# Performance work log

Measured on AMD Instinct MI355X. Metric: run time of the kernel, lower is better.

## Reference

```python
import jax, jax.numpy as jnp
import numpy as np

B, S, H = 128, 512, 512  # batch, seq_len, hidden_units; feature dim is 2H = 1024
D = 2 * H


def setup_inputs() -> dict:
    key = jax.random.key(0)
    ks = jax.random.split(key, 8)
    scale = 1.0 / np.sqrt(D)
    return {
        "h_dec": jax.random.normal(ks[0], (1, B, H), jnp.float32),
        "c_dec": jax.random.normal(ks[1], (1, B, H), jnp.float32),
        "encoder_output": jax.random.normal(ks[2], (B, S, D), jnp.float32),
        "x_padding_masks": jnp.ones((B, S), jnp.float32),
        "coverage_vector": jax.random.uniform(ks[3], (B, S), jnp.float32),
        "Wh_w": jax.random.normal(ks[4], (D, D), jnp.float32) * scale,
        "Ws_w": jax.random.normal(ks[5], (D, D), jnp.float32) * scale,
        "Ws_b": jax.random.normal(ks[6], (D,), jnp.float32) * scale,
        "v_w": jax.random.normal(ks[7], (D,), jnp.float32) * scale,
        "wc_w": jax.random.normal(jax.random.fold_in(key, 99), (D,), jnp.float32) * scale,
    }


def reference(h_dec, c_dec, encoder_output, x_padding_masks, coverage_vector,
              Wh_w, Ws_w, Ws_b, v_w, wc_w):
    # s_t: concat(h, c) -> (B, 2H)
    s_t = jnp.concatenate([h_dec[0], c_dec[0]], axis=-1)  # (B, D)
    enc_feat = jnp.einsum('bsd,ed->bse', encoder_output, Wh_w)       # Wh(enc)
    dec_feat = s_t @ Ws_w.T + Ws_b                                    # (B, D)
    cov_feat = coverage_vector[:, :, None] * wc_w[None, None, :]      # w_c(cov)
    att_inputs = enc_feat + dec_feat[:, None, :] + cov_feat           # (B, S, D)
    score = jnp.tanh(att_inputs) @ v_w                                # (B, S)
    aw = jax.nn.softmax(score, axis=1) * x_padding_masks              # masked softmax
    aw = aw / jnp.sum(aw, axis=1, keepdims=True)                      # renormalize
    context_vector = jnp.einsum('bs,bsd->bd', aw, encoder_output)     # (B, D)
    new_coverage = coverage_vector + aw
    return context_vector, aw, new_coverage
```

## Files before the change

### kernel.cpp

```cpp
#include <hip/hip_runtime.h>
#include <hip/hip_bf16.h>
#include <cstdint>
#include <cstddef>


typedef __attribute__((ext_vector_type(8))) short bf16x8;
typedef __attribute__((ext_vector_type(4))) float f32x4;

#define GLOBAL_AS(p) ((const __attribute__((address_space(1))) unsigned int*)(p))
#define LDS_AS(p)    ((__attribute__((address_space(3))) unsigned int*)(p))

__device__ __forceinline__ short f2bf(float f) {
    union { float f; uint32_t u; } v; v.f = f;
    uint32_t u = v.u + 0x7fffu + ((v.u >> 16) & 1u);
    return (short)(u >> 16);
}

__device__ __forceinline__ float bf2f(short s) {
    union { uint32_t u; float f; } v; v.u = ((uint32_t)(uint16_t)s) << 16;
    return v.f;
}

__device__ __forceinline__ bf16x8 cvt8(float4 a, float4 b) {
    bf16x8 r;
    r[0] = f2bf(a.x); r[1] = f2bf(a.y); r[2] = f2bf(a.z); r[3] = f2bf(a.w);
    r[4] = f2bf(b.x); r[5] = f2bf(b.y); r[6] = f2bf(b.z); r[7] = f2bf(b.w);
    return r;
}

__device__ __forceinline__ float fast_tanh(float x) {
    x = fminf(10.f, fmaxf(-10.f, x));
    float e = __expf(2.f * x);
    return (e - 1.f) / (e + 1.f);
}

__device__ __forceinline__ float fast_tanh2(float x) {
    float e = __builtin_amdgcn_exp2f(x * 2.885390081777927f);
    return 1.f - 2.f * __builtin_amdgcn_rcpf(e + 1.f);
}

__global__ __launch_bounds__(256) void cvt_plus_dec(
    const float* __restrict__ enc, const float* __restrict__ Wh,
    short* __restrict__ enc_bf, short* __restrict__ Wh_bf,
    const float* __restrict__ hd, const float* __restrict__ cd,
    const float* __restrict__ Ws, float* __restrict__ dec_part)
{
    __shared__ __align__(16) short As[128 * 40];
    __shared__ __align__(16) short Bs[128 * 40];
    const int t = threadIdx.x;

    if (blockIdx.x < 33280) {
        size_t i = ((size_t)blockIdx.x * 256 + t) * 8;
        const float* src; short* dst; size_t off;
        const size_t NE = 67108864;
        if (i < NE) { src = enc; dst = enc_bf; off = i; }
        else        { src = Wh;  dst = Wh_bf;  off = i - NE; }
        float4 a = *(const float4*)(src + off);
        float4 b = *(const float4*)(src + off + 4);
        *(bf16x8*)(dst + off) = cvt8(a, b);
        return;
    }

    const int bid = blockIdx.x - 33280;
    const int bx = bid & 7;
    const int kc = bid >> 3;
    const int wv = t >> 6, lane = t & 63, q = lane >> 4, c = lane & 15;
    const int wm = wv & 1, wn = wv >> 1;
    const int ar = t >> 1, ah = t & 1;

    const float* abase = ((kc < 2) ? hd : cd) + (size_t)ar * 512 + (kc & 1) * 256 + ah * 16;
    const float* bbase = Ws + ((size_t)(bx * 128 + ar)) * 1024 + kc * 256 + ah * 16;
    short* awr = &As[ar * 40 + ah * 16];
    short* bwr = &Bs[ar * 40 + ah * 16];

    f32x4 acc[4][4];
#pragma unroll
    for (int i = 0; i < 4; ++i)
#pragma unroll
        for (int j = 0; j < 4; ++j) acc[i][j] = (f32x4){0.f, 0.f, 0.f, 0.f};

    for (int k0 = 0; k0 < 256; k0 += 32) {
        const float4* ap = (const float4*)(abase + k0);
        const float4* bp = (const float4*)(bbase + k0);
        float4 a0 = ap[0], a1 = ap[1], a2 = ap[2], a3 = ap[3];
        float4 b0 = bp[0], b1 = bp[1], b2 = bp[2], b3 = bp[3];
        *(bf16x8*)awr = cvt8(a0, a1);
        *(bf16x8*)(awr + 8) = cvt8(a2, a3);
        *(bf16x8*)bwr = cvt8(b0, b1);
        *(bf16x8*)(bwr + 8) = cvt8(b2, b3);
        __syncthreads();
        bf16x8 af[4], bf[4];
#pragma unroll
        for (int i = 0; i < 4; ++i) af[i] = *(const bf16x8*)&As[(wm * 64 + i * 16 + c) * 40 + q * 8];
#pragma unroll
        for (int j = 0; j < 4; ++j) bf[j] = *(const bf16x8*)&Bs[(wn * 64 + j * 16 + c) * 40 + q * 8];
#pragma unroll
        for (int i = 0; i < 4; ++i)
#pragma unroll
            for (int j = 0; j < 4; ++j)
                acc[i][j] = __builtin_amdgcn_mfma_f32_16x16x32_bf16(af[i], bf[j], acc[i][j], 0, 0, 0);
        __syncthreads();
    }

    const int n0 = bx * 128 + wn * 64;
    float* dp = dec_part + (size_t)kc * 131072;
#pragma unroll
    for (int i = 0; i < 4; ++i)
#pragma unroll
        for (int rr = 0; rr < 4; ++rr) {
            int bidx = wm * 64 + i * 16 + q * 4 + rr;
#pragma unroll
            for (int j = 0; j < 4; ++j)
                dp[(size_t)bidx * 1024 + n0 + j * 16 + c] = acc[i][j][rr];
        }
}


#define BARRIER() do { asm volatile("" ::: "memory"); \
    __builtin_amdgcn_s_barrier(); asm volatile("" ::: "memory"); } while (0)
#define WAIT_LGKM0() do { asm volatile("s_waitcnt lgkmcnt(0)" ::: "memory"); \
    __builtin_amdgcn_sched_barrier(0); } while (0)
#define STAGE(gp, kcol, arr, bufks, a) \
    __builtin_amdgcn_global_load_lds(GLOBAL_AS((gp) + (kcol)), \
        LDS_AS(&(arr)[(bufks) * 8192 + (a) * 4096 + wst]), 16, 0, 0)

__global__ __launch_bounds__(512, 2) void attn_score_gemm8(
    const short* __restrict__ encb, const short* __restrict__ Whb,
    const float* __restrict__ dec_part, const float* __restrict__ Wsb,
    const float* __restrict__ cov,
    const float* __restrict__ wc_w, const float* __restrict__ v_w,
    float* __restrict__ p_part)
{
    __shared__ __align__(16) short SA[32768];
    __shared__ __align__(16) short SB[32768];

    const int tid = threadIdx.x;
    const int wv = tid >> 6, lane = tid & 63, q = lane >> 4, c = lane & 15;
    const int wm = wv >> 2, wn = wv & 3;

    const int lin = blockIdx.x;
    const int xcd = lin & 7;
    const int idx = lin >> 3;
    const int bx  = idx & 3;
    const int my  = xcd * 32 + (idx >> 2);
    const int m0  = my * 256;
    const int n0  = bx * 256;
    const int b   = my >> 1;
    const int s0c = (my & 1) * 256;

    const int srow = tid >> 2;
    const int SLOT = ((tid & 3) ^ ((tid >> 3) & 3)) * 8;
    const short* gA0 = encb + (size_t)(m0 + srow) * 1024 + SLOT;
    const short* gA1 = gA0 + 131072;
    const short* gB0 = Whb + (size_t)(n0 + srow) * 1024 + SLOT;
    const short* gB1 = gB0 + 131072;
    const int wst = wv * 512;

    const int sq = (q ^ ((c >> 1) & 3)) * 8;
    int aoff[8], boff[4];
#pragma unroll
    for (int i = 0; i < 8; ++i) aoff[i] = (wm * 128 + i * 16 + c) * 32 + sq;
#pragma unroll
    for (int j = 0; j < 4; ++j) boff[j] = (wn * 64 + j * 16 + c) * 32 + sq;

    f32x4 acc[8][4];
#pragma unroll
    for (int i = 0; i < 8; ++i)
#pragma unroll
        for (int j = 0; j < 4; ++j) acc[i][j] = (f32x4){0.f, 0.f, 0.f, 0.f};

    STAGE(gA0,  0, SA, 0, 0);  STAGE(gA1,  0, SA, 0, 1);
    STAGE(gB0,  0, SB, 0, 0);  STAGE(gB1,  0, SB, 0, 1);
    STAGE(gA0, 32, SA, 1, 0);  STAGE(gA1, 32, SA, 1, 1);
    STAGE(gB0, 32, SB, 1, 0);  STAGE(gB1, 32, SB, 1, 1);
    STAGE(gA0, 64, SA, 2, 0);  STAGE(gA1, 64, SA, 2, 1);
    STAGE(gB0, 64, SB, 2, 0);  STAGE(gB1, 64, SB, 2, 1);
    asm volatile("s_waitcnt vmcnt(4)" ::: "memory");
    __builtin_amdgcn_s_barrier();
    asm volatile("" ::: "memory");

#pragma unroll 2
    for (int t = 0; t < 16; ++t) {
        const int cur = t & 1, nxt = cur ^ 1;
        const int kc = t * 64;
        const short* A0 = &SA[cur * 16384];
        const short* A1 = A0 + 8192;
        const short* B0 = &SB[cur * 16384];
        const short* B1 = B0 + 8192;

        bf16x8 af[4], bfr[4];

#pragma unroll
        for (int i = 0; i < 4; ++i) af[i] = *(const bf16x8*)&A0[aoff[i]];
#pragma unroll
        for (int j = 0; j < 4; ++j) bfr[j] = *(const bf16x8*)&B0[boff[j]];
        if (t < 15) { STAGE(gA0, kc + 96, SA, nxt * 2 + 1, 0);
                      STAGE(gA1, kc + 96, SA, nxt * 2 + 1, 1); }
        WAIT_LGKM0();
        __builtin_amdgcn_s_setprio(1);
#pragma unroll
        for (int i = 0; i < 4; ++i)
#pragma unroll
            for (int j = 0; j < 4; ++j)
                acc[i][j] = __builtin_amdgcn_mfma_f32_16x16x32_bf16(af[i], bfr[j], acc[i][j], 0, 0, 0);
        __builtin_amdgcn_s_setprio(0);

#pragma unroll
        for (int i = 0; i < 4; ++i) af[i] = *(const bf16x8*)&A0[aoff[4 + i]];
        if (t < 15) { STAGE(gB0, kc + 96, SB, nxt * 2 + 1, 0);
                      STAGE(gB1, kc + 96, SB, nxt * 2 + 1, 1); }
        WAIT_LGKM0();
        __builtin_amdgcn_s_setprio(1);
#pragma unroll
        for (int i = 0; i < 4; ++i)
#pragma unroll
            for (int j = 0; j < 4; ++j)
                acc[4 + i][j] = __builtin_amdgcn_mfma_f32_16x16x32_bf16(af[i], bfr[j], acc[4 + i][j], 0, 0, 0);
        __builtin_amdgcn_s_setprio(0);
        BARRIER();

#pragma unroll
        for (int i = 0; i < 4; ++i) af[i] = *(const bf16x8*)&A1[aoff[i]];
#pragma unroll
        for (int j = 0; j < 4; ++j) bfr[j] = *(const bf16x8*)&B1[boff[j]];
        if (t < 14) { STAGE(gA0, kc + 128, SA, cur * 2, 0);
                      STAGE(gA1, kc + 128, SA, cur * 2, 1); }
        WAIT_LGKM0();
        __builtin_amdgcn_s_setprio(1);
#pragma unroll
        for (int i = 0; i < 4; ++i)
#pragma unroll
            for (int j = 0; j < 4; ++j)
                acc[i][j] = __builtin_amdgcn_mfma_f32_16x16x32_bf16(af[i], bfr[j], acc[i][j], 0, 0, 0);
        __builtin_amdgcn_s_setprio(0);

#pragma unroll
        for (int i = 0; i < 4; ++i) af[i] = *(const bf16x8*)&A1[aoff[4 + i]];
        if (t < 14) { STAGE(gB0, kc + 128, SB, cur * 2, 0);
                      STAGE(gB1, kc + 128, SB, cur * 2, 1); }
        WAIT_LGKM0();
        __builtin_amdgcn_s_setprio(1);
#pragma unroll
        for (int i = 0; i < 4; ++i)
#pragma unroll
            for (int j = 0; j < 4; ++j)
                acc[4 + i][j] = __builtin_amdgcn_mfma_f32_16x16x32_bf16(af[i], bfr[j], acc[4 + i][j], 0, 0, 0);
        __builtin_amdgcn_s_setprio(0);
        if (t <= 13) asm volatile("s_waitcnt vmcnt(4)" ::: "memory");
        else         asm volatile("s_waitcnt vmcnt(0)" ::: "memory");
        __builtin_amdgcn_s_barrier();
        asm volatile("" ::: "memory");
    }

    const int eb = n0 + wn * 64;
    float v_e[4], wc_e[4], dec_e[4];
#pragma unroll
    for (int j = 0; j < 4; ++j) {
        int e = eb + j * 16 + c;
        v_e[j]  = v_w[e];
        wc_e[j] = wc_w[e];
        float d = Wsb[e];
#pragma unroll
        for (int p = 0; p < 4; ++p) d += dec_part[(size_t)p * 131072 + (size_t)b * 1024 + e];
        dec_e[j] = d;
    }
    const float* covb = cov + (size_t)b * 512 + s0c;
    float* pp = p_part + (size_t)(bx * 4 + wn) * 65536 + (size_t)my * 256;
#pragma unroll
    for (int i = 0; i < 8; ++i)
#pragma unroll
        for (int rr = 0; rr < 4; ++rr) {
            int r = wm * 128 + i * 16 + q * 4 + rr;
            float cs = covb[r];
            float p = 0.f;
#pragma unroll
            for (int j = 0; j < 4; ++j) {
                float att = acc[i][j][rr] + dec_e[j] + cs * wc_e[j];
                p += v_e[j] * fast_tanh2(att);
            }
            p += __shfl_xor(p, 1);
            p += __shfl_xor(p, 2);
            p += __shfl_xor(p, 4);
            p += __shfl_xor(p, 8);
            if (c == 0) pp[r] = p;
        }
}

__global__ __launch_bounds__(256) void attn_score_gemm_fb(
    const float* __restrict__ enc, const short* __restrict__ Wh,
    const float* __restrict__ dec_feat, const float* __restrict__ cov,
    const float* __restrict__ wc_w, const float* __restrict__ v_w,
    float* __restrict__ p_part)
{
    __shared__ __align__(16) short As[128 * 40];
    __shared__ __align__(16) short Bs[128 * 40];
    const int t = threadIdx.x;
    const int bx = blockIdx.x;
    const int by = blockIdx.y;
    const int b  = by >> 2;
    const int s0 = (by & 3) * 128;

    const int wv = t >> 6, lane = t & 63, q = lane >> 4, c = lane & 15;
    const int wm = wv & 1, wn = wv >> 1;
    const int ar = t >> 1, ah = t & 1;

    const float* aptr = enc + ((size_t)(by * 128 + ar)) * 1024 + ah * 16;
    const short* bptr = Wh + ((size_t)(bx * 128 + ar)) * 1024 + ah * 16;
    short* awr = &As[ar * 40 + ah * 16];
    short* bwr = &Bs[ar * 40 + ah * 16];

    f32x4 acc[4][4];
#pragma unroll
    for (int i = 0; i < 4; ++i)
#pragma unroll
        for (int j = 0; j < 4; ++j) acc[i][j] = (f32x4){0.f, 0.f, 0.f, 0.f};

    for (int k0 = 0; k0 < 1024; k0 += 32) {
        const float4* ap = (const float4*)(aptr + k0);
        float4 a0 = ap[0], a1 = ap[1], a2 = ap[2], a3 = ap[3];
        bf16x8 bv0 = *(const bf16x8*)(bptr + k0);
        bf16x8 bv1 = *(const bf16x8*)(bptr + k0 + 8);
        *(bf16x8*)awr = cvt8(a0, a1);
        *(bf16x8*)(awr + 8) = cvt8(a2, a3);
        *(bf16x8*)bwr = bv0;
        *(bf16x8*)(bwr + 8) = bv1;
        __syncthreads();
        bf16x8 af[4], bf[4];
#pragma unroll
        for (int i = 0; i < 4; ++i) af[i] = *(const bf16x8*)&As[(wm * 64 + i * 16 + c) * 40 + q * 8];
#pragma unroll
        for (int j = 0; j < 4; ++j) bf[j] = *(const bf16x8*)&Bs[(wn * 64 + j * 16 + c) * 40 + q * 8];
#pragma unroll
        for (int i = 0; i < 4; ++i)
#pragma unroll
            for (int j = 0; j < 4; ++j)
                acc[i][j] = __builtin_amdgcn_mfma_f32_16x16x32_bf16(af[i], bf[j], acc[i][j], 0, 0, 0);
        __syncthreads();
    }

    const int n0 = bx * 128 + wn * 64;
    float v_e[4], wc_e[4], dec_e[4];
#pragma unroll
    for (int j = 0; j < 4; ++j) {
        int e = n0 + j * 16 + c;
        v_e[j]  = v_w[e];
        wc_e[j] = wc_w[e];
        dec_e[j] = dec_feat[(size_t)b * 1024 + e];
    }
    const float* covb = cov + (size_t)b * 512;
    float* pp = p_part + ((size_t)(bx * 2 + wn)) * 65536 + (size_t)b * 512;
#pragma unroll
    for (int i = 0; i < 4; ++i)
#pragma unroll
        for (int rr = 0; rr < 4; ++rr) {
            int s = s0 + wm * 64 + i * 16 + q * 4 + rr;
            float cs = covb[s];
            float p = 0.f;
#pragma unroll
            for (int j = 0; j < 4; ++j) {
                float att = acc[i][j][rr] + dec_e[j] + cs * wc_e[j];
                p += v_e[j] * fast_tanh(att);
            }
            p += __shfl_xor(p, 1);
            p += __shfl_xor(p, 2);
            p += __shfl_xor(p, 4);
            p += __shfl_xor(p, 8);
            if (c == 0) pp[s] = p;
        }
}

__global__ __launch_bounds__(256) void dec_gemm(
    const float* __restrict__ hd, const float* __restrict__ cd,
    const short* __restrict__ Ws, const float* __restrict__ Wsb,
    float* __restrict__ dec_feat)
{
    __shared__ __align__(16) short As[128 * 40];
    __shared__ __align__(16) short Bs[128 * 40];
    const int t = threadIdx.x;
    const int bx = blockIdx.x;
    const int wv = t >> 6, lane = t & 63, q = lane >> 4, c = lane & 15;
    const int wm = wv & 1, wn = wv >> 1;
    const int ar = t >> 1, ah = t & 1;

    const short* bptr = Ws + ((size_t)(bx * 128 + ar)) * 1024 + ah * 16;
    short* awr = &As[ar * 40 + ah * 16];
    short* bwr = &Bs[ar * 40 + ah * 16];

    f32x4 acc[4][4];
#pragma unroll
    for (int i = 0; i < 4; ++i)
#pragma unroll
        for (int j = 0; j < 4; ++j) acc[i][j] = (f32x4){0.f, 0.f, 0.f, 0.f};

    for (int k0 = 0; k0 < 1024; k0 += 32) {
        const int k = k0 + ah * 16;
        const float* src = (k < 512) ? (hd + (size_t)ar * 512 + k)
                                     : (cd + (size_t)ar * 512 + (k - 512));
        const float4* ap = (const float4*)src;
        float4 a0 = ap[0], a1 = ap[1], a2 = ap[2], a3 = ap[3];
        bf16x8 bv0 = *(const bf16x8*)(bptr + k0);
        bf16x8 bv1 = *(const bf16x8*)(bptr + k0 + 8);
        *(bf16x8*)awr = cvt8(a0, a1);
        *(bf16x8*)(awr + 8) = cvt8(a2, a3);
        *(bf16x8*)bwr = bv0;
        *(bf16x8*)(bwr + 8) = bv1;
        __syncthreads();
        bf16x8 af[4], bf[4];
#pragma unroll
        for (int i = 0; i < 4; ++i) af[i] = *(const bf16x8*)&As[(wm * 64 + i * 16 + c) * 40 + q * 8];
#pragma unroll
        for (int j = 0; j < 4; ++j) bf[j] = *(const bf16x8*)&Bs[(wn * 64 + j * 16 + c) * 40 + q * 8];
#pragma unroll
        for (int i = 0; i < 4; ++i)
#pragma unroll
            for (int j = 0; j < 4; ++j)
                acc[i][j] = __builtin_amdgcn_mfma_f32_16x16x32_bf16(af[i], bf[j], acc[i][j], 0, 0, 0);
        __syncthreads();
    }

    const int n0 = bx * 128 + wn * 64;
    float wsb_e[4];
#pragma unroll
    for (int j = 0; j < 4; ++j) wsb_e[j] = Wsb[n0 + j * 16 + c];
#pragma unroll
    for (int i = 0; i < 4; ++i)
#pragma unroll
        for (int rr = 0; rr < 4; ++rr) {
            int bidx = wm * 64 + i * 16 + q * 4 + rr;
#pragma unroll
            for (int j = 0; j < 4; ++j) {
                int e = n0 + j * 16 + c;
                dec_feat[(size_t)bidx * 1024 + e] = acc[i][j][rr] + wsb_e[j];
            }
        }
}

__global__ __launch_bounds__(512) void softmax_kernel(
    const float* __restrict__ p_part, int ns, const float* __restrict__ mask,
    const float* __restrict__ cov, float* __restrict__ aw, float* __restrict__ ncov)
{
    __shared__ float red[8];
    const int b = blockIdx.x, t = threadIdx.x;
    const int w = t >> 6, lane = t & 63;
    const size_t idx = (size_t)b * 512 + t;

    float sc = 0.f;
    for (int k = 0; k < ns; ++k) sc += p_part[(size_t)k * 65536 + idx];

    float m = sc;
#pragma unroll
    for (int o = 1; o < 64; o <<= 1) m = fmaxf(m, __shfl_xor(m, o));
    if (lane == 0) red[w] = m;
    __syncthreads();
#pragma unroll
    for (int i = 0; i < 8; ++i) m = fmaxf(m, red[i]);
    __syncthreads();

    float e = __expf(sc - m);
    float s = e;
#pragma unroll
    for (int o = 1; o < 64; o <<= 1) s += __shfl_xor(s, o);
    if (lane == 0) red[w] = s;
    __syncthreads();
    s = 0.f;
#pragma unroll
    for (int i = 0; i < 8; ++i) s += red[i];
    __syncthreads();

    float wv = (e / s) * mask[idx];
    float s2 = wv;
#pragma unroll
    for (int o = 1; o < 64; o <<= 1) s2 += __shfl_xor(s2, o);
    if (lane == 0) red[w] = s2;
    __syncthreads();
    s2 = 0.f;
#pragma unroll
    for (int i = 0; i < 8; ++i) s2 += red[i];

    float awv = wv / s2;
    aw[idx] = awv;
    ncov[idx] = cov[idx] + awv;
}

__global__ __launch_bounds__(256) void context_part(
    const short* __restrict__ encb, const float* __restrict__ aw, float* __restrict__ cpart)
{
    const int sc = blockIdx.x & 7;
    const int b  = blockIdx.x >> 3;
    const int t  = threadIdx.x;
    const int dl = t & 127;
    const int si = t >> 7;
    const short* ebase = encb + ((size_t)(b * 512 + sc * 64 + si)) * 1024 + dl * 8;
    const float* awp = aw + (size_t)b * 512 + sc * 64 + si;
    float acc[8];
#pragma unroll
    for (int i = 0; i < 8; ++i) acc[i] = 0.f;
#pragma unroll 16
    for (int s = 0; s < 64; s += 2) {
        float w = awp[s];
        bf16x8 e = *(const bf16x8*)(ebase + (size_t)s * 1024);
#pragma unroll
        for (int i = 0; i < 8; ++i) acc[i] += w * bf2f(e[i]);
    }
    float* cp = cpart + ((size_t)(sc * 2 + si) * 128 + b) * 1024 + dl * 8;
    *(float4*)(cp)     = (float4){acc[0], acc[1], acc[2], acc[3]};
    *(float4*)(cp + 4) = (float4){acc[4], acc[5], acc[6], acc[7]};
}

__global__ __launch_bounds__(256) void ctx_reduce(
    const float* __restrict__ cpart, float* __restrict__ ctx)
{
    int i = blockIdx.x * 256 + threadIdx.x;
    float s = 0.f;
#pragma unroll
    for (int k = 0; k < 16; ++k) s += cpart[(size_t)k * 131072 + i];
    ctx[i] = s;
}

__global__ __launch_bounds__(256) void context_f32(
    const float* __restrict__ enc, const float* __restrict__ aw, float* __restrict__ ctx)
{
    const int schunk = blockIdx.x;
    const int b = blockIdx.y;
    const int t = threadIdx.x;
    const float* ebase = enc + ((size_t)(b * 512 + schunk * 128)) * 1024 + t * 4;
    const float* awp = aw + (size_t)b * 512 + schunk * 128;
    float ax = 0.f, ay = 0.f, az = 0.f, aww = 0.f;
#pragma unroll 4
    for (int s = 0; s < 128; ++s) {
        float w = awp[s];
        float4 e4 = *(const float4*)(ebase + (size_t)s * 1024);
        ax += w * e4.x; ay += w * e4.y; az += w * e4.z; aww += w * e4.w;
    }
    float* cp = ctx + (size_t)b * 1024 + t * 4;
    atomicAdd(cp + 0, ax);
    atomicAdd(cp + 1, ay);
    atomicAdd(cp + 2, az);
    atomicAdd(cp + 3, aww);
}

__global__ void cvt_f32_bf16(const float* __restrict__ src, short* __restrict__ dst, int n) {
    int i = (blockIdx.x * 256 + threadIdx.x) * 4;
    if (i < n) {
        float4 f = *(const float4*)(src + i);
        short4 o;
        o.x = f2bf(f.x); o.y = f2bf(f.y); o.z = f2bf(f.z); o.w = f2bf(f.w);
        *(short4*)(dst + i) = o;
    }
}

extern "C" void kernel_launch(void* const* d_in, const int* in_sizes, int n_in,
                              void* d_out, int out_size, void* d_ws, size_t ws_size,
                              hipStream_t stream) {
    const float* hd   = (const float*)d_in[0];
    const float* cd   = (const float*)d_in[1];
    const float* enc  = (const float*)d_in[2];
    const float* mask = (const float*)d_in[3];
    const float* cov  = (const float*)d_in[4];
    const float* Wh   = (const float*)d_in[5];
    const float* Ws   = (const float*)d_in[6];
    const float* Wsb  = (const float*)d_in[7];
    const float* vw   = (const float*)d_in[8];
    const float* wcw  = (const float*)d_in[9];

    float* out  = (float*)d_out;
    float* ctx  = out;
    float* aw   = out + 131072;
    float* ncov = out + 196608;

    char* ws = (char*)d_ws;
    float* p_part   = (float*)ws;
    float* dec_part = (float*)(ws + (4u << 20));
    short* Wh_bf    = (short*)(ws + (6u << 20));
    short* enc_bf   = (short*)(ws + (8u << 20));
    float* cpart    = (float*)ws;
    const size_t need_big = (8ull << 20) + (128ull << 20);

    if (ws_size >= need_big) {
        cvt_plus_dec<<<33312, 256, 0, stream>>>(enc, Wh, enc_bf, Wh_bf, hd, cd, Ws, dec_part);
        attn_score_gemm8<<<1024, 512, 0, stream>>>(enc_bf, Wh_bf, dec_part, Wsb, cov, wcw, vw, p_part);
        softmax_kernel<<<128, 512, 0, stream>>>(p_part, 16, mask, cov, aw, ncov);
        context_part<<<1024, 256, 0, stream>>>(enc_bf, aw, cpart);
        ctx_reduce<<<512, 256, 0, stream>>>(cpart, ctx);
    } else {
        float* p_part16 = (float*)ws;
        float* dec_feat = (float*)(ws + (4u << 20));
        short* Wh_bf2   = (short*)(ws + (4u << 20) + (512u << 10));
        short* Ws_bf    = (short*)(ws + (6u << 20) + (512u << 10));
        hipMemsetAsync(ctx, 0, 128 * 1024 * sizeof(float), stream);
        cvt_f32_bf16<<<1024, 256, 0, stream>>>(Wh, Wh_bf2, 1024 * 1024);
        cvt_f32_bf16<<<1024, 256, 0, stream>>>(Ws, Ws_bf, 1024 * 1024);
        dec_gemm<<<8, 256, 0, stream>>>(hd, cd, Ws_bf, Wsb, dec_feat);
        attn_score_gemm_fb<<<dim3(8, 512), 256, 0, stream>>>(enc, Wh_bf2, dec_feat, cov, wcw, vw, p_part16);
        softmax_kernel<<<128, 512, 0, stream>>>(p_part16, 16, mask, cov, aw, ncov);
        context_f32<<<dim3(4, 128), 256, 0, stream>>>(enc, aw, ctx);
    }
}
```

Before: 583.5 us.

## Replace 4-stage LDS pipeline with simple double buffer to raise occupancy

Rewrites the main score GEMM loop from a 4-slot, 64-wide k-step pipeline with interleaved half-stages into a plain double buffer over 32-wide k-slices, with one barrier per slice. LDS use per block is halved and launch bounds ask for 4 blocks per CU instead of 2, aiming to hide latency through more resident waves rather than deep software prefetch. In exchange each iteration waits for all outstanding global loads (vmcnt(0)) before its barrier, so there is less prefetch depth and more barriers. With 8x4 f32x4 accumulators per thread, the register cap implied by 4 blocks of 512 threads may cause spills.

```diff
diff --git a/kernel.cpp b/kernel.cpp
--- a/kernel.cpp
+++ b/kernel.cpp
@@ -116,23 +116,21 @@
 }
 
 
-#define BARRIER() do { asm volatile("" ::: "memory"); \
-    __builtin_amdgcn_s_barrier(); asm volatile("" ::: "memory"); } while (0)
 #define WAIT_LGKM0() do { asm volatile("s_waitcnt lgkmcnt(0)" ::: "memory"); \
     __builtin_amdgcn_sched_barrier(0); } while (0)
-#define STAGE(gp, kcol, arr, bufks, a) \
+#define STAGE9(gp, kcol, arr, slot, a) \
     __builtin_amdgcn_global_load_lds(GLOBAL_AS((gp) + (kcol)), \
-        LDS_AS(&(arr)[(bufks) * 8192 + (a) * 4096 + wst]), 16, 0, 0)
-
-__global__ __launch_bounds__(512, 2) void attn_score_gemm8(
+        LDS_AS(&(arr)[(slot) * 8192 + (a) * 4096 + wst]), 16, 0, 0)
+
+__global__ __launch_bounds__(512, 4) void attn_score_gemm9(
     const short* __restrict__ encb, const short* __restrict__ Whb,
     const float* __restrict__ dec_part, const float* __restrict__ Wsb,
     const float* __restrict__ cov,
     const float* __restrict__ wc_w, const float* __restrict__ v_w,
     float* __restrict__ p_part)
 {
-    __shared__ __align__(16) short SA[32768];
-    __shared__ __align__(16) short SB[32768];
+    __shared__ __align__(16) short SA[16384];
+    __shared__ __align__(16) short SB[16384];
 
     const int tid = threadIdx.x;
     const int wv = tid >> 6, lane = tid & 63, q = lane >> 4, c = lane & 15;
@@ -169,85 +167,36 @@
 #pragma unroll
         for (int j = 0; j < 4; ++j) acc[i][j] = (f32x4){0.f, 0.f, 0.f, 0.f};
 
-    STAGE(gA0,  0, SA, 0, 0);  STAGE(gA1,  0, SA, 0, 1);
-    STAGE(gB0,  0, SB, 0, 0);  STAGE(gB1,  0, SB, 0, 1);
-    STAGE(gA0, 32, SA, 1, 0);  STAGE(gA1, 32, SA, 1, 1);
-    STAGE(gB0, 32, SB, 1, 0);  STAGE(gB1, 32, SB, 1, 1);
-    STAGE(gA0, 64, SA, 2, 0);  STAGE(gA1, 64, SA, 2, 1);
-    STAGE(gB0, 64, SB, 2, 0);  STAGE(gB1, 64, SB, 2, 1);
-    asm volatile("s_waitcnt vmcnt(4)" ::: "memory");
+    STAGE9(gA0, 0, SA, 0, 0);  STAGE9(gA1, 0, SA, 0, 1);
+    STAGE9(gB0, 0, SB, 0, 0);  STAGE9(gB1, 0, SB, 0, 1);
+    asm volatile("s_waitcnt vmcnt(0)" ::: "memory");
     __builtin_amdgcn_s_barrier();
     asm volatile("" ::: "memory");
 
 #pragma unroll 2
-    for (int t = 0; t < 16; ++t) {
-        const int cur = t & 1, nxt = cur ^ 1;
-        const int kc = t * 64;
-        const short* A0 = &SA[cur * 16384];
-        const short* A1 = A0 + 8192;
-        const short* B0 = &SB[cur * 16384];
-        const short* B1 = B0 + 8192;
-
-        bf16x8 af[4], bfr[4];
-
-#pragma unroll
-        for (int i = 0; i < 4; ++i) af[i] = *(const bf16x8*)&A0[aoff[i]];
-#pragma unroll
-        for (int j = 0; j < 4; ++j) bfr[j] = *(const bf16x8*)&B0[boff[j]];
-        if (t < 15) { STAGE(gA0, kc + 96, SA, nxt * 2 + 1, 0);
-                      STAGE(gA1, kc + 96, SA, nxt * 2 + 1, 1); }
+    for (int kh = 0; kh < 32; ++kh) {
+        const int slot = kh & 1, nslot = slot ^ 1;
+        if (kh < 31) {
+            const int kcol = (kh + 1) * 32;
+            STAGE9(gA0, kcol, SA, nslot, 0);  STAGE9(gA1, kcol, SA, nslot, 1);
+            STAGE9(gB0, kcol, SB, nslot, 0);  STAGE9(gB1, kcol, SB, nslot, 1);
+        }
+        const short* A = &SA[slot * 8192];
+        const short* B = &SB[slot * 8192];
+        bf16x8 af[8], bfr[4];
+#pragma unroll
+        for (int i = 0; i < 8; ++i) af[i] = *(const bf16x8*)&A[aoff[i]];
+#pragma unroll
+        for (int j = 0; j < 4; ++j) bfr[j] = *(const bf16x8*)&B[boff[j]];
         WAIT_LGKM0();
         __builtin_amdgcn_s_setprio(1);
 #pragma unroll
-        for (int i = 0; i < 4; ++i)
+        for (int i = 0; i < 8; ++i)
 #pragma unroll
             for (int j = 0; j < 4; ++j)
                 acc[i][j] = __builtin_amdgcn_mfma_f32_16x16x32_bf16(af[i], bfr[j], acc[i][j], 0, 0, 0);
         __builtin_amdgcn_s_setprio(0);
-
-#pragma unroll
-        for (int i = 0; i < 4; ++i) af[i] = *(const bf16x8*)&A0[aoff[4 + i]];
-        if (t < 15) { STAGE(gB0, kc + 96, SB, nxt * 2 + 1, 0);
-                      STAGE(gB1, kc + 96, SB, nxt * 2 + 1, 1); }
-        WAIT_LGKM0();
-        __builtin_amdgcn_s_setprio(1);
-#pragma unroll
-        for (int i = 0; i < 4; ++i)
-#pragma unroll
-            for (int j = 0; j < 4; ++j)
-                acc[4 + i][j] = __builtin_amdgcn_mfma_f32_16x16x32_bf16(af[i], bfr[j], acc[4 + i][j], 0, 0, 0);
-        __builtin_amdgcn_s_setprio(0);
-        BARRIER();
-
-#pragma unroll
-        for (int i = 0; i < 4; ++i) af[i] = *(const bf16x8*)&A1[aoff[i]];
-#pragma unroll
-        for (int j = 0; j < 4; ++j) bfr[j] = *(const bf16x8*)&B1[boff[j]];
-        if (t < 14) { STAGE(gA0, kc + 128, SA, cur * 2, 0);
-                      STAGE(gA1, kc + 128, SA, cur * 2, 1); }
-        WAIT_LGKM0();
-        __builtin_amdgcn_s_setprio(1);
-#pragma unroll
-        for (int i = 0; i < 4; ++i)
-#pragma unroll
-            for (int j = 0; j < 4; ++j)
-                acc[i][j] = __builtin_amdgcn_mfma_f32_16x16x32_bf16(af[i], bfr[j], acc[i][j], 0, 0, 0);
-        __builtin_amdgcn_s_setprio(0);
-
-#pragma unroll
-        for (int i = 0; i < 4; ++i) af[i] = *(const bf16x8*)&A1[aoff[4 + i]];
-        if (t < 14) { STAGE(gB0, kc + 128, SB, cur * 2, 0);
-                      STAGE(gB1, kc + 128, SB, cur * 2, 1); }
-        WAIT_LGKM0();
-        __builtin_amdgcn_s_setprio(1);
-#pragma unroll
-        for (int i = 0; i < 4; ++i)
-#pragma unroll
-            for (int j = 0; j < 4; ++j)
-                acc[4 + i][j] = __builtin_amdgcn_mfma_f32_16x16x32_bf16(af[i], bfr[j], acc[4 + i][j], 0, 0, 0);
-        __builtin_amdgcn_s_setprio(0);
-        if (t <= 13) asm volatile("s_waitcnt vmcnt(4)" ::: "memory");
-        else         asm volatile("s_waitcnt vmcnt(0)" ::: "memory");
+        asm volatile("s_waitcnt vmcnt(0)" ::: "memory");
         __builtin_amdgcn_s_barrier();
         asm volatile("" ::: "memory");
     }
@@ -578,7 +527,7 @@
 
     if (ws_size >= need_big) {
         cvt_plus_dec<<<33312, 256, 0, stream>>>(enc, Wh, enc_bf, Wh_bf, hd, cd, Ws, dec_part);
-        attn_score_gemm8<<<1024, 512, 0, stream>>>(enc_bf, Wh_bf, dec_part, Wsb, cov, wcw, vw, p_part);
+        attn_score_gemm9<<<1024, 512, 0, stream>>>(enc_bf, Wh_bf, dec_part, Wsb, cov, wcw, vw, p_part);
         softmax_kernel<<<128, 512, 0, stream>>>(p_part, 16, mask, cov, aw, ncov);
         context_part<<<1024, 256, 0, stream>>>(enc_bf, aw, cpart);
         ctx_reduce<<<512, 256, 0, stream>>>(cpart, ctx);
```

Result: slower. 1.839 ms (+215.1%).

## Fuse encoder fp32-to-bf16 conversion into score GEMM A-tile loading

Applied to the files above, without the earlier changes.

Drops the separate pass that converted the whole encoder tensor to bf16 in workspace. The score GEMM now loads fp32 encoder rows into registers, converts them, and writes bf16 to LDS inside its software pipeline, while the B tiles still use direct global-to-LDS loads. The context kernel now reads the fp32 encoder directly. This avoids writing and re-reading a 128MB bf16 copy and reduces workspace needs, but doubles the A-operand global traffic in the GEMM, adds conversion ALU work and register pressure, and changes the pipeline's wait and barrier structure.

```diff
diff --git a/kernel.cpp b/kernel.cpp
--- a/kernel.cpp
+++ b/kernel.cpp
@@ -39,9 +39,8 @@
     return 1.f - 2.f * __builtin_amdgcn_rcpf(e + 1.f);
 }
 
-__global__ __launch_bounds__(256) void cvt_plus_dec(
-    const float* __restrict__ enc, const float* __restrict__ Wh,
-    short* __restrict__ enc_bf, short* __restrict__ Wh_bf,
+__global__ __launch_bounds__(256) void dec_cvt(
+    const float* __restrict__ Wh, short* __restrict__ Wh_bf,
     const float* __restrict__ hd, const float* __restrict__ cd,
     const float* __restrict__ Ws, float* __restrict__ dec_part)
 {
@@ -49,19 +48,15 @@
     __shared__ __align__(16) short Bs[128 * 40];
     const int t = threadIdx.x;
 
-    if (blockIdx.x < 33280) {
+    if (blockIdx.x < 512) {
         size_t i = ((size_t)blockIdx.x * 256 + t) * 8;
-        const float* src; short* dst; size_t off;
-        const size_t NE = 67108864;
-        if (i < NE) { src = enc; dst = enc_bf; off = i; }
-        else        { src = Wh;  dst = Wh_bf;  off = i - NE; }
-        float4 a = *(const float4*)(src + off);
-        float4 b = *(const float4*)(src + off + 4);
-        *(bf16x8*)(dst + off) = cvt8(a, b);
+        float4 a = *(const float4*)(Wh + i);
+        float4 b = *(const float4*)(Wh + i + 4);
+        *(bf16x8*)(Wh_bf + i) = cvt8(a, b);
         return;
     }
 
-    const int bid = blockIdx.x - 33280;
+    const int bid = blockIdx.x - 512;
     const int bx = bid & 7;
     const int kc = bid >> 3;
     const int wv = t >> 6, lane = t & 63, q = lane >> 4, c = lane & 15;
@@ -116,16 +111,14 @@
 }
 
 
-#define BARRIER() do { asm volatile("" ::: "memory"); \
-    __builtin_amdgcn_s_barrier(); asm volatile("" ::: "memory"); } while (0)
 #define WAIT_LGKM0() do { asm volatile("s_waitcnt lgkmcnt(0)" ::: "memory"); \
     __builtin_amdgcn_sched_barrier(0); } while (0)
 #define STAGE(gp, kcol, arr, bufks, a) \
     __builtin_amdgcn_global_load_lds(GLOBAL_AS((gp) + (kcol)), \
         LDS_AS(&(arr)[(bufks) * 8192 + (a) * 4096 + wst]), 16, 0, 0)
 
-__global__ __launch_bounds__(512, 2) void attn_score_gemm8(
-    const short* __restrict__ encb, const short* __restrict__ Whb,
+__global__ __launch_bounds__(512, 2) void attn_score_gemm11(
+    const float* __restrict__ encf, const short* __restrict__ Whb,
     const float* __restrict__ dec_part, const float* __restrict__ Wsb,
     const float* __restrict__ cov,
     const float* __restrict__ wc_w, const float* __restrict__ v_w,
@@ -150,12 +143,17 @@
 
     const int srow = tid >> 2;
     const int SLOT = ((tid & 3) ^ ((tid >> 3) & 3)) * 8;
-    const short* gA0 = encb + (size_t)(m0 + srow) * 1024 + SLOT;
-    const short* gA1 = gA0 + 131072;
     const short* gB0 = Whb + (size_t)(n0 + srow) * 1024 + SLOT;
     const short* gB1 = gB0 + 131072;
     const int wst = wv * 512;
 
+    const int ar2 = tid >> 1;
+    const int as2 = (tid & 1) * 2;
+    const int ag  = as2 ^ ((ar2 >> 1) & 3);
+    const float* gAf  = encf + (size_t)(m0 + ar2) * 1024 + ag * 8;
+    const float* gAf2 = encf + (size_t)(m0 + ar2) * 1024 + (ag ^ 1) * 8;
+    const int wrA = ar2 * 32 + as2 * 8;
+
     const int sq = (q ^ ((c >> 1) & 3)) * 8;
     int aoff[8], boff[4];
 #pragma unroll
@@ -169,20 +167,31 @@
 #pragma unroll
         for (int j = 0; j < 4; ++j) acc[i][j] = (f32x4){0.f, 0.f, 0.f, 0.f};
 
-    STAGE(gA0,  0, SA, 0, 0);  STAGE(gA1,  0, SA, 0, 1);
+    float4 aR0, aR1, aR2, aR3, aR4, aR5, aR6, aR7;
+    aR0 = *(const float4*)(gAf);        aR1 = *(const float4*)(gAf + 4);
+    aR2 = *(const float4*)(gAf2);       aR3 = *(const float4*)(gAf2 + 4);
+    aR4 = *(const float4*)(gAf + 32);   aR5 = *(const float4*)(gAf + 36);
+    aR6 = *(const float4*)(gAf2 + 32);  aR7 = *(const float4*)(gAf2 + 36);
     STAGE(gB0,  0, SB, 0, 0);  STAGE(gB1,  0, SB, 0, 1);
-    STAGE(gA0, 32, SA, 1, 0);  STAGE(gA1, 32, SA, 1, 1);
     STAGE(gB0, 32, SB, 1, 0);  STAGE(gB1, 32, SB, 1, 1);
-    STAGE(gA0, 64, SA, 2, 0);  STAGE(gA1, 64, SA, 2, 1);
-    STAGE(gB0, 64, SB, 2, 0);  STAGE(gB1, 64, SB, 2, 1);
     asm volatile("s_waitcnt vmcnt(4)" ::: "memory");
+    {
+        short* w0 = &SA[wrA];
+        *(bf16x8*)w0        = cvt8(aR0, aR1);
+        *(bf16x8*)(w0 + 8)  = cvt8(aR2, aR3);
+        short* w1 = w0 + 8192;
+        *(bf16x8*)w1        = cvt8(aR4, aR5);
+        *(bf16x8*)(w1 + 8)  = cvt8(aR6, aR7);
+    }
+    asm volatile("s_waitcnt vmcnt(0)" ::: "memory");
+    asm volatile("s_waitcnt lgkmcnt(0)" ::: "memory");
     __builtin_amdgcn_s_barrier();
     asm volatile("" ::: "memory");
 
 #pragma unroll 2
     for (int t = 0; t < 16; ++t) {
         const int cur = t & 1, nxt = cur ^ 1;
-        const int kc = t * 64;
+        const int kb = (t + 1) * 64;
         const short* A0 = &SA[cur * 16384];
         const short* A1 = A0 + 8192;
         const short* B0 = &SB[cur * 16384];
@@ -194,8 +203,12 @@
         for (int i = 0; i < 4; ++i) af[i] = *(const bf16x8*)&A0[aoff[i]];
 #pragma unroll
         for (int j = 0; j < 4; ++j) bfr[j] = *(const bf16x8*)&B0[boff[j]];
-        if (t < 15) { STAGE(gA0, kc + 96, SA, nxt * 2 + 1, 0);
-                      STAGE(gA1, kc + 96, SA, nxt * 2 + 1, 1); }
+        if (t < 15) {
+            aR0 = *(const float4*)(gAf + kb);        aR1 = *(const float4*)(gAf + kb + 4);
+            aR2 = *(const float4*)(gAf2 + kb);       aR3 = *(const float4*)(gAf2 + kb + 4);
+            aR4 = *(const float4*)(gAf + kb + 32);   aR5 = *(const float4*)(gAf + kb + 36);
+            aR6 = *(const float4*)(gAf2 + kb + 32);  aR7 = *(const float4*)(gAf2 + kb + 36);
+        }
         WAIT_LGKM0();
         __builtin_amdgcn_s_setprio(1);
 #pragma unroll
@@ -207,8 +220,12 @@
 
 #pragma unroll
         for (int i = 0; i < 4; ++i) af[i] = *(const bf16x8*)&A0[aoff[4 + i]];
-        if (t < 15) { STAGE(gB0, kc + 96, SB, nxt * 2 + 1, 0);
-                      STAGE(gB1, kc + 96, SB, nxt * 2 + 1, 1); }
+        if (t < 15) {
+            STAGE(gB0, kb,      SB, nxt * 2,     0);
+            STAGE(gB1, kb,      SB, nxt * 2,     1);
+            STAGE(gB0, kb + 32, SB, nxt * 2 + 1, 0);
+            STAGE(gB1, kb + 32, SB, nxt * 2 + 1, 1);
+        }
         WAIT_LGKM0();
         __builtin_amdgcn_s_setprio(1);
 #pragma unroll
@@ -217,14 +234,20 @@
             for (int j = 0; j < 4; ++j)
                 acc[4 + i][j] = __builtin_amdgcn_mfma_f32_16x16x32_bf16(af[i], bfr[j], acc[4 + i][j], 0, 0, 0);
         __builtin_amdgcn_s_setprio(0);
-        BARRIER();
 
 #pragma unroll
         for (int i = 0; i < 4; ++i) af[i] = *(const bf16x8*)&A1[aoff[i]];
 #pragma unroll
         for (int j = 0; j < 4; ++j) bfr[j] = *(const bf16x8*)&B1[boff[j]];
-        if (t < 14) { STAGE(gA0, kc + 128, SA, cur * 2, 0);
-                      STAGE(gA1, kc + 128, SA, cur * 2, 1); }
+        if (t < 15) {
+            asm volatile("s_waitcnt vmcnt(4)" ::: "memory");
+            short* w0 = &SA[nxt * 16384 + wrA];
+            *(bf16x8*)w0        = cvt8(aR0, aR1);
+            *(bf16x8*)(w0 + 8)  = cvt8(aR2, aR3);
+            short* w1 = w0 + 8192;
+            *(bf16x8*)w1        = cvt8(aR4, aR5);
+            *(bf16x8*)(w1 + 8)  = cvt8(aR6, aR7);
+        }
         WAIT_LGKM0();
         __builtin_amdgcn_s_setprio(1);
 #pragma unroll
@@ -236,8 +259,6 @@
 
 #pragma unroll
         for (int i = 0; i < 4; ++i) af[i] = *(const bf16x8*)&A1[aoff[4 + i]];
-        if (t < 14) { STAGE(gB0, kc + 128, SB, cur * 2, 0);
-                      STAGE(gB1, kc + 128, SB, cur * 2, 1); }
         WAIT_LGKM0();
         __builtin_amdgcn_s_setprio(1);
 #pragma unroll
@@ -246,8 +267,7 @@
             for (int j = 0; j < 4; ++j)
                 acc[4 + i][j] = __builtin_amdgcn_mfma_f32_16x16x32_bf16(af[i], bfr[j], acc[4 + i][j], 0, 0, 0);
         __builtin_amdgcn_s_setprio(0);
-        if (t <= 13) asm volatile("s_waitcnt vmcnt(4)" ::: "memory");
-        else         asm volatile("s_waitcnt vmcnt(0)" ::: "memory");
+        asm volatile("s_waitcnt vmcnt(0)" ::: "memory");
         __builtin_amdgcn_s_barrier();
         asm volatile("" ::: "memory");
     }
@@ -284,6 +304,89 @@
             p += __shfl_xor(p, 8);
             if (c == 0) pp[r] = p;
         }
+}
+
+__global__ __launch_bounds__(512) void softmax_kernel(
+    const float* __restrict__ p_part, int ns, const float* __restrict__ mask,
+    const float* __restrict__ cov, float* __restrict__ aw, float* __restrict__ ncov)
+{
+    __shared__ float red[8];
+    const int b = blockIdx.x, t = threadIdx.x;
+    const int w = t >> 6, lane = t & 63;
+    const size_t idx = (size_t)b * 512 + t;
+
+    float sc = 0.f;
+    for (int k = 0; k < ns; ++k) sc += p_part[(size_t)k * 65536 + idx];
+
+    float m = sc;
+#pragma unroll
+    for (int o = 1; o < 64; o <<= 1) m = fmaxf(m, __shfl_xor(m, o));
+    if (lane == 0) red[w] = m;
+    __syncthreads();
+#pragma unroll
+    for (int i = 0; i < 8; ++i) m = fmaxf(m, red[i]);
+    __syncthreads();
+
+    float e = __expf(sc - m);
+    float s = e;
+#pragma unroll
+    for (int o = 1; o < 64; o <<= 1) s += __shfl_xor(s, o);
+    if (lane == 0) red[w] = s;
+    __syncthreads();
+    s = 0.f;
+#pragma unroll
+    for (int i = 0; i < 8; ++i) s += red[i];
+    __syncthreads();
+
+    float wv = (e / s) * mask[idx];
+    float s2 = wv;
+#pragma unroll
+    for (int o = 1; o < 64; o <<= 1) s2 += __shfl_xor(s2, o);
+    if (lane == 0) red[w] = s2;
+    __syncthreads();
+    s2 = 0.f;
+#pragma unroll
+    for (int i = 0; i < 8; ++i) s2 += red[i];
+
+    float awv = wv / s2;
+    aw[idx] = awv;
+    ncov[idx] = cov[idx] + awv;
+}
+
+__global__ __launch_bounds__(256) void context_part_f32(
+    const float* __restrict__ enc, const float* __restrict__ aw, float* __restrict__ cpart)
+{
+    const int sc = blockIdx.x & 7;
+    const int b  = blockIdx.x >> 3;
+    const int t  = threadIdx.x;
+    const int dl = t & 127;
+    const int si = t >> 7;
+    const float* ebase = enc + ((size_t)(b * 512 + sc * 64 + si)) * 1024 + dl * 8;
+    const float* awp = aw + (size_t)b * 512 + sc * 64 + si;
+    float acc[8];
+#pragma unroll
+    for (int i = 0; i < 8; ++i) acc[i] = 0.f;
+#pragma unroll 8
+    for (int s = 0; s < 64; s += 2) {
+        float w = awp[s];
+        float4 e0 = *(const float4*)(ebase + (size_t)s * 1024);
+        float4 e1 = *(const float4*)(ebase + (size_t)s * 1024 + 4);
+        acc[0] += w * e0.x; acc[1] += w * e0.y; acc[2] += w * e0.z; acc[3] += w * e0.w;
+        acc[4] += w * e1.x; acc[5] += w * e1.y; acc[6] += w * e1.z; acc[7] += w * e1.w;
+    }
+    float* cp = cpart + ((size_t)(sc * 2 + si) * 128 + b) * 1024 + dl * 8;
+    *(float4*)(cp)     = (float4){acc[0], acc[1], acc[2], acc[3]};
+    *(float4*)(cp + 4) = (float4){acc[4], acc[5], acc[6], acc[7]};
+}
+
+__global__ __launch_bounds__(256) void ctx_reduce(
+    const float* __restrict__ cpart, float* __restrict__ ctx)
+{
+    int i = blockIdx.x * 256 + threadIdx.x;
+    float s = 0.f;
+#pragma unroll
+    for (int k = 0; k < 16; ++k) s += cpart[(size_t)k * 131072 + i];
+    ctx[i] = s;
 }
 
 __global__ __launch_bounds__(256) void attn_score_gemm_fb(
@@ -435,88 +538,6 @@
         }
 }
 
-__global__ __launch_bounds__(512) void softmax_kernel(
-    const float* __restrict__ p_part, int ns, const float* __restrict__ mask,
-    const float* __restrict__ cov, float* __restrict__ aw, float* __restrict__ ncov)
-{
-    __shared__ float red[8];
-    const int b = blockIdx.x, t = threadIdx.x;
-    const int w = t >> 6, lane = t & 63;
-    const size_t idx = (size_t)b * 512 + t;
-
-    float sc = 0.f;
-    for (int k = 0; k < ns; ++k) sc += p_part[(size_t)k * 65536 + idx];
-
-    float m = sc;
-#pragma unroll
-    for (int o = 1; o < 64; o <<= 1) m = fmaxf(m, __shfl_xor(m, o));
-    if (lane == 0) red[w] = m;
-    __syncthreads();
-#pragma unroll
-    for (int i = 0; i < 8; ++i) m = fmaxf(m, red[i]);
-    __syncthreads();
-
-    float e = __expf(sc - m);
-    float s = e;
-#pragma unroll
-    for (int o = 1; o < 64; o <<= 1) s += __shfl_xor(s, o);
-    if (lane == 0) red[w] = s;
-    __syncthreads();
-    s = 0.f;
-#pragma unroll
-    for (int i = 0; i < 8; ++i) s += red[i];
-    __syncthreads();
-
-    float wv = (e / s) * mask[idx];
-    float s2 = wv;
-#pragma unroll
-    for (int o = 1; o < 64; o <<= 1) s2 += __shfl_xor(s2, o);
-    if (lane == 0) red[w] = s2;
-    __syncthreads();
-    s2 = 0.f;
-#pragma unroll
-    for (int i = 0; i < 8; ++i) s2 += red[i];
-
-    float awv = wv / s2;
-    aw[idx] = awv;
-    ncov[idx] = cov[idx] + awv;
-}
-
-__global__ __launch_bounds__(256) void context_part(
-    const short* __restrict__ encb, const float* __restrict__ aw, float* __restrict__ cpart)
-{
-    const int sc = blockIdx.x & 7;
-    const int b  = blockIdx.x >> 3;
-    const int t  = threadIdx.x;
-    const int dl = t & 127;
-    const int si = t >> 7;
-    const short* ebase = encb + ((size_t)(b * 512 + sc * 64 + si)) * 1024 + dl * 8;
-    const float* awp = aw + (size_t)b * 512 + sc * 64 + si;
-    float acc[8];
-#pragma unroll
-    for (int i = 0; i < 8; ++i) acc[i] = 0.f;
-#pragma unroll 16
-    for (int s = 0; s < 64; s += 2) {
-        float w = awp[s];
-        bf16x8 e = *(const bf16x8*)(ebase + (size_t)s * 1024);
-#pragma unroll
-        for (int i = 0; i < 8; ++i) acc[i] += w * bf2f(e[i]);
-    }
-    float* cp = cpart + ((size_t)(sc * 2 + si) * 128 + b) * 1024 + dl * 8;
-    *(float4*)(cp)     = (float4){acc[0], acc[1], acc[2], acc[3]};
-    *(float4*)(cp + 4) = (float4){acc[4], acc[5], acc[6], acc[7]};
-}
-
-__global__ __launch_bounds__(256) void ctx_reduce(
-    const float* __restrict__ cpart, float* __restrict__ ctx)
-{
-    int i = blockIdx.x * 256 + threadIdx.x;
-    float s = 0.f;
-#pragma unroll
-    for (int k = 0; k < 16; ++k) s += cpart[(size_t)k * 131072 + i];
-    ctx[i] = s;
-}
-
 __global__ __launch_bounds__(256) void context_f32(
     const float* __restrict__ enc, const float* __restrict__ aw, float* __restrict__ ctx)
 {
@@ -572,15 +593,14 @@
     float* p_part   = (float*)ws;
     float* dec_part = (float*)(ws + (4u << 20));
     short* Wh_bf    = (short*)(ws + (6u << 20));
-    short* enc_bf   = (short*)(ws + (8u << 20));
     float* cpart    = (float*)ws;
-    const size_t need_big = (8ull << 20) + (128ull << 20);
+    const size_t need_big = (16ull << 20);
 
     if (ws_size >= need_big) {
-        cvt_plus_dec<<<33312, 256, 0, stream>>>(enc, Wh, enc_bf, Wh_bf, hd, cd, Ws, dec_part);
-        attn_score_gemm8<<<1024, 512, 0, stream>>>(enc_bf, Wh_bf, dec_part, Wsb, cov, wcw, vw, p_part);
+        dec_cvt<<<544, 256, 0, stream>>>(Wh, Wh_bf, hd, cd, Ws, dec_part);
+        attn_score_gemm11<<<1024, 512, 0, stream>>>(enc, Wh_bf, dec_part, Wsb, cov, wcw, vw, p_part);
         softmax_kernel<<<128, 512, 0, stream>>>(p_part, 16, mask, cov, aw, ncov);
-        context_part<<<1024, 256, 0, stream>>>(enc_bf, aw, cpart);
+        context_part_f32<<<1024, 256, 0, stream>>>(enc, aw, cpart);
         ctx_reduce<<<512, 256, 0, stream>>>(cpart, ctx);
     } else {
         float* p_part16 = (float*)ws;
```

After: 611.7 us. 4.8% more time.
